# Optimization experiments

Hardware: AMD Instinct MI355X
Metric: run time of the kernel (lower is better)

The kernel has to match this reference:

```python
import jax, jax.numpy as jnp
import numpy as np

B = 32768
D_IN = 512
UNITS = 512


def setup_inputs() -> dict:
    key = jax.random.key(0)
    ks = jax.random.split(key, 12)
    s = 1.0 / np.sqrt(D_IN)
    sh = 1.0 / np.sqrt(UNITS)
    return {
        "inputs": jax.random.normal(ks[0], (B, D_IN), dtype=jnp.float32),
        "state": jax.random.normal(ks[1], (B, UNITS), dtype=jnp.float32),
        "att_score": jax.random.uniform(ks[2], (B, 1), dtype=jnp.float32),
        # update gate
        "Wu_x": jax.random.normal(ks[3], (D_IN, UNITS), dtype=jnp.float32) * s,
        "bu": jnp.zeros((UNITS,), dtype=jnp.float32),
        "Wu_h": jax.random.normal(ks[4], (UNITS, UNITS), dtype=jnp.float32) * sh,
        # reset gate
        "Wr_x": jax.random.normal(ks[5], (D_IN, UNITS), dtype=jnp.float32) * s,
        "br": jnp.zeros((UNITS,), dtype=jnp.float32),
        "Wr_h": jax.random.normal(ks[6], (UNITS, UNITS), dtype=jnp.float32) * sh,
        # candidate memory
        "Wc_x": jax.random.normal(ks[7], (D_IN, UNITS), dtype=jnp.float32) * s,
        "bc": jnp.zeros((UNITS,), dtype=jnp.float32),
        "Wc_h": jax.random.normal(ks[8], (UNITS, UNITS), dtype=jnp.float32) * sh,
    }


def reference(inputs, state, att_score, Wu_x, bu, Wu_h, Wr_x, br, Wr_h, Wc_x, bc, Wc_h):
    # u = sigmoid(Dense_act(x) + Dense_noact(h))
    u = jax.nn.sigmoid(inputs @ Wu_x + bu + state @ Wu_h)
    # r = sigmoid(Dense_act(x) + Dense_noact(h))
    r = jax.nn.sigmoid(inputs @ Wr_x + br + state @ Wr_h)
    # c = tanh(Dense_act(x) + r * Dense_noact(h))
    c = jnp.tanh(inputs @ Wc_x + bc + r * (state @ Wc_h))
    u_ = att_score * u  # [B,1] * [B,U] broadcast
    state_next = (1.0 - u_) * state + u_ * c
    return state_next
```

## Files before the change

### kernel.cpp

```cpp
#include <hip/hip_runtime.h>
#include <hip/hip_bf16.h>
#include <stdint.h>

#define B_ROWS 32768
#define DIM 512
#define THREADS 256
#define NKT 32
#define ASLOT 16384
#define LDS_TOTAL (3 * ASLOT)

typedef __attribute__((ext_vector_type(8))) __bf16 bf16x8;
typedef __attribute__((ext_vector_type(4))) float f32x4;
typedef __attribute__((ext_vector_type(4))) unsigned int uint4v;

__device__ static inline unsigned short f2bf(float f) {
    unsigned int u = __builtin_bit_cast(unsigned int, f);
    u += 0x7fffu + ((u >> 16) & 1u);
    return (unsigned short)(u >> 16);
}

__device__ static inline void load_lds_16B(const void* g, void* lds) {
    __builtin_amdgcn_global_load_lds(
        (const __attribute__((address_space(1))) unsigned int*)g,
        (__attribute__((address_space(3))) unsigned int*)lds,
        16, 0, 0);
}

__global__ void prep_weights(const float* __restrict__ Wu_x, const float* __restrict__ Wu_h,
                             const float* __restrict__ Wr_x, const float* __restrict__ Wr_h,
                             const float* __restrict__ Wc_x, const float* __restrict__ Wc_h,
                             unsigned short* __restrict__ Wt2) {
    __shared__ float tile[32][33];
    const int t = blockIdx.z;
    const int k0 = blockIdx.x * 32;
    const int n0 = blockIdx.y * 32;
    const float* Wx = (t == 0) ? Wu_x : (t == 1) ? Wr_x : Wc_x;
    const float* Wh = (t == 0) ? Wu_h : (t == 1) ? Wr_h : Wc_h;
    const int tid = threadIdx.x;
    const int c = tid & 31, r0 = tid >> 5;
#pragma unroll
    for (int i = 0; i < 4; ++i) {
        int kl = r0 + i * 8;
        int k = k0 + kl;
        int n = n0 + c;
        float v = (k < 512) ? Wx[(size_t)k * 512 + n] : Wh[(size_t)(k - 512) * 512 + n];
        tile[kl][c] = v;
    }
    __syncthreads();
    const int kt = k0 >> 5;
#pragma unroll
    for (int i = 0; i < 4; ++i) {
        int nl = r0 + i * 8;
        int kc = c;
        int n = n0 + nl;
        Wt2[(((size_t)kt * 3 + t) * 512 + n) * 32 + kc] = f2bf(tile[kc][nl]);
    }
}

__global__ __launch_bounds__(THREADS, 2) void augru_main(
    const float* __restrict__ x, const float* __restrict__ h,
    const float* __restrict__ att, const unsigned short* __restrict__ Wt2,
    const float* __restrict__ bu, const float* __restrict__ br,
    const float* __restrict__ bc, float* __restrict__ out) {
    extern __shared__ char smem[];
    const int tid = threadIdx.x;
    const int lane = tid & 63;
    const int wid = tid >> 6;
    const int wm = wid >> 1;
    const int wn = wid & 1;
    const int id = blockIdx.x;
    const int wg = (id & 7) * 256 + (id >> 3);
    const int nb = wg & 7;
    const int mb = wg >> 3;
    const int cl = lane & 15;
    const int kg = lane >> 4;

    f32x4 accU[4][2], accR[4][2], accCx[4][2], accCh[4][2];
#pragma unroll
    for (int i = 0; i < 4; ++i)
#pragma unroll
        for (int j = 0; j < 2; ++j) {
            accU[i][j] = (f32x4)(0.f);
            accR[i][j] = (f32x4)(0.f);
            accCx[i][j] = (f32x4)(0.f);
            accCh[i][j] = (f32x4)(0.f);
        }

    const int arow_l = lane >> 3;
    const int ag = lane & 7;
    const unsigned aoffBase =
        (unsigned)(mb * 128 + wid * 32 + arow_l) * 2048
        + (unsigned)((ag * 16) ^ (arow_l << 4));
    auto stageA = [&](int slot, int ktn) {
        const char* bp = (ktn < 16) ? (const char*)x : (const char*)h;
        const unsigned ko = (unsigned)(ktn & 15) * 128;
        char* ldsb = smem + slot * ASLOT + wid * 4096;
#pragma unroll
        for (int q = 0; q < 4; ++q)
            load_lds_16B(bp + aoffBase + q * 16384 + ko, ldsb + q * 1024);
    };

    const char* gW = (const char*)Wt2
        + (size_t)((nb * 64 + wn * 32 + cl) * 64 + kg * 16);
    bf16x8 bbA[3][2], bbB[3][2];
    auto loadW = [&](bf16x8(&dst)[3][2], int ktn) {
        const char* p = gW + (size_t)ktn * 98304;
#pragma unroll
        for (int t = 0; t < 3; ++t)
#pragma unroll
            for (int ni = 0; ni < 2; ++ni)
                dst[t][ni] = *(const bf16x8*)(p + t * 32768 + ni * 1024);
    };

    auto cvt2 = [](float lo, float hi) {
        unsigned int r;
        asm("v_cvt_pk_bf16_f32 %0, %1, %2" : "=v"(r) : "v"(lo), "v"(hi));
        return r;
    };

    const int s7 = cl & 7;
    const int aRd1 = (wm * 64 + cl) * 128 + (((kg * 2) ^ s7) * 16);
    const int aRd2 = (wm * 64 + cl) * 128 + (((kg * 2 + 1) ^ s7) * 16);
    auto readA = [&](int slot, int mi) {
        const char* p = smem + slot * ASLOT + mi * 2048;
        f32x4 lo = *(const f32x4*)(p + aRd1);
        f32x4 hi = *(const f32x4*)(p + aRd2);
        uint4v q;
        q.x = cvt2(lo[0], lo[1]); q.y = cvt2(lo[2], lo[3]);
        q.z = cvt2(hi[0], hi[1]); q.w = cvt2(hi[2], hi[3]);
        return __builtin_bit_cast(bf16x8, q);
    };

    stageA(0, 0);
    stageA(1, 1);
    loadW(bbA, 0);

    auto body = [&](int kt, bf16x8(&cur)[3][2], bf16x8(&nxt)[3][2],
                    f32x4(&accC)[4][2]) {
        asm volatile("s_waitcnt vmcnt(0)" ::: "memory");
        __builtin_amdgcn_s_barrier();
        if (kt + 2 < NKT) stageA((kt + 2) % 3, kt + 2);
        if (kt + 1 < NKT) loadW(nxt, kt + 1);
        __builtin_amdgcn_sched_barrier(0);
        const int slot = kt % 3;
        bf16x8 a[4];
#pragma unroll
        for (int mi = 0; mi < 4; ++mi)
            a[mi] = readA(slot, mi);
        __builtin_amdgcn_s_setprio(1);
#pragma unroll
        for (int ni = 0; ni < 2; ++ni) {
#pragma unroll
            for (int mi = 0; mi < 4; ++mi)
                accU[mi][ni] = __builtin_amdgcn_mfma_f32_16x16x32_bf16(
                    a[mi], cur[0][ni], accU[mi][ni], 0, 0, 0);
#pragma unroll
            for (int mi = 0; mi < 4; ++mi)
                accR[mi][ni] = __builtin_amdgcn_mfma_f32_16x16x32_bf16(
                    a[mi], cur[1][ni], accR[mi][ni], 0, 0, 0);
#pragma unroll
            for (int mi = 0; mi < 4; ++mi)
                accC[mi][ni] = __builtin_amdgcn_mfma_f32_16x16x32_bf16(
                    a[mi], cur[2][ni], accC[mi][ni], 0, 0, 0);
        }
        __builtin_amdgcn_s_setprio(0);
    };

    body(0, bbA, bbB, accCx);  body(1, bbB, bbA, accCx);
    body(2, bbA, bbB, accCx);  body(3, bbB, bbA, accCx);
    body(4, bbA, bbB, accCx);  body(5, bbB, bbA, accCx);
    body(6, bbA, bbB, accCx);  body(7, bbB, bbA, accCx);
    body(8, bbA, bbB, accCx);  body(9, bbB, bbA, accCx);
    body(10, bbA, bbB, accCx); body(11, bbB, bbA, accCx);
    body(12, bbA, bbB, accCx); body(13, bbB, bbA, accCx);
    body(14, bbA, bbB, accCx); body(15, bbB, bbA, accCx);
    body(16, bbA, bbB, accCh); body(17, bbB, bbA, accCh);
    body(18, bbA, bbB, accCh); body(19, bbB, bbA, accCh);
    body(20, bbA, bbB, accCh); body(21, bbB, bbA, accCh);
    body(22, bbA, bbB, accCh); body(23, bbB, bbA, accCh);
    body(24, bbA, bbB, accCh); body(25, bbB, bbA, accCh);
    body(26, bbA, bbB, accCh); body(27, bbB, bbA, accCh);
    body(28, bbA, bbB, accCh); body(29, bbB, bbA, accCh);
    body(30, bbA, bbB, accCh); body(31, bbB, bbA, accCh);

#pragma unroll
    for (int ni = 0; ni < 2; ++ni) {
        const int col = nb * 64 + wn * 32 + ni * 16 + cl;
        const float bU = bu[col];
        const float bR = br[col];
        const float bC = bc[col];
#pragma unroll
        for (int mi = 0; mi < 4; ++mi) {
#pragma unroll
            for (int j = 0; j < 4; ++j) {
                const int row = mb * 128 + wm * 64 + mi * 16 + kg * 4 + j;
                const float up = accU[mi][ni][j] + bU;
                const float rp = accR[mi][ni][j] + bR;
                const float u = 1.f / (1.f + __expf(-up));
                const float r = 1.f / (1.f + __expf(-rp));
                const float cpre = accCx[mi][ni][j] + bC + r * accCh[mi][ni][j];
                const float e = __expf(-2.f * cpre);
                const float cc = (1.f - e) / (1.f + e);
                const float aa = att[row];
                const float hv = h[(size_t)row * 512 + col];
                const float u_ = aa * u;
                out[(size_t)row * 512 + col] = (1.f - u_) * hv + u_ * cc;
            }
        }
    }
}

extern "C" void kernel_launch(void* const* d_in, const int* in_sizes, int n_in,
                              void* d_out, int out_size, void* d_ws, size_t ws_size,
                              hipStream_t stream) {
    const float* x    = (const float*)d_in[0];
    const float* h    = (const float*)d_in[1];
    const float* att  = (const float*)d_in[2];
    const float* Wu_x = (const float*)d_in[3];
    const float* bu   = (const float*)d_in[4];
    const float* Wu_h = (const float*)d_in[5];
    const float* Wr_x = (const float*)d_in[6];
    const float* br   = (const float*)d_in[7];
    const float* Wr_h = (const float*)d_in[8];
    const float* Wc_x = (const float*)d_in[9];
    const float* bc   = (const float*)d_in[10];
    const float* Wc_h = (const float*)d_in[11];
    unsigned short* Wt2 = (unsigned short*)d_ws;
    float* out = (float*)d_out;

    prep_weights<<<dim3(32, 16, 3), 256, 0, stream>>>(Wu_x, Wu_h, Wr_x, Wr_h, Wc_x, Wc_h, Wt2);

    hipFuncSetAttribute((const void*)augru_main,
                        hipFuncAttributeMaxDynamicSharedMemorySize, LDS_TOTAL);
    augru_main<<<dim3(2048), THREADS, LDS_TOTAL, stream>>>(
        x, h, att, Wt2, bu, br, bc, out);
}
```

Baseline: 158.8 us.

## Stage A tiles through registers, convert to bf16 before LDS write

The fp32 activation tiles are no longer copied straight into LDS with global_load_lds. Each thread now loads them into registers, converts them to bf16 once, and writes the bf16 data to a double-buffered LDS slot with a new swizzle. This halves LDS footprint and LDS read traffic, and removes the repeated per-wave fp32-to-bf16 conversion when reading A. In exchange it costs extra VGPRs for the in-flight loads, adds a register round trip, and reduces the pipeline depth from three stages to two.

```diff
diff --git a/kernel.cpp b/kernel.cpp
--- a/kernel.cpp
+++ b/kernel.cpp
@@ -6,8 +6,8 @@
 #define DIM 512
 #define THREADS 256
 #define NKT 32
-#define ASLOT 16384
-#define LDS_TOTAL (3 * ASLOT)
+#define ASLOT 8192
+#define LDS_TOTAL (2 * ASLOT)
 
 typedef __attribute__((ext_vector_type(8))) __bf16 bf16x8;
 typedef __attribute__((ext_vector_type(4))) float f32x4;
@@ -17,13 +17,6 @@
     unsigned int u = __builtin_bit_cast(unsigned int, f);
     u += 0x7fffu + ((u >> 16) & 1u);
     return (unsigned short)(u >> 16);
-}
-
-__device__ static inline void load_lds_16B(const void* g, void* lds) {
-    __builtin_amdgcn_global_load_lds(
-        (const __attribute__((address_space(1))) unsigned int*)g,
-        (__attribute__((address_space(3))) unsigned int*)lds,
-        16, 0, 0);
 }
 
 __global__ void prep_weights(const float* __restrict__ Wu_x, const float* __restrict__ Wu_h,
@@ -86,30 +79,43 @@
             accCh[i][j] = (f32x4)(0.f);
         }
 
-    const int arow_l = lane >> 3;
-    const int ag = lane & 7;
-    const unsigned aoffBase =
-        (unsigned)(mb * 128 + wid * 32 + arow_l) * 2048
-        + (unsigned)((ag * 16) ^ (arow_l << 4));
-    auto stageA = [&](int slot, int ktn) {
-        const char* bp = (ktn < 16) ? (const char*)x : (const char*)h;
-        const unsigned ko = (unsigned)(ktn & 15) * 128;
-        char* ldsb = smem + slot * ASLOT + wid * 4096;
-#pragma unroll
-        for (int q = 0; q < 4; ++q)
-            load_lds_16B(bp + aoffBase + q * 16384 + ko, ldsb + q * 1024);
+    const int rowb = wm * 64 + cl;
+    const int aBase = rowb * 64 + ((kg * 16) ^ (((rowb >> 1) & 3) << 4));
+
+    const int arow = tid >> 1;
+    const int ap = tid & 1;
+    const int asw = ((arow >> 1) & 3) << 4;
+    const int dsA0 = arow * 64 + ((ap * 32) ^ asw);
+    const int dsA1 = arow * 64 + ((ap * 32 + 16) ^ asw);
+    const float* pAx = x + (size_t)(mb * 128 + arow) * 512 + ap * 16;
+    const float* pAh = h + (size_t)(mb * 128 + arow) * 512 - 512 + ap * 16;
+
+    f32x4 fa[4];
+    auto issueA = [&](int ktn) {
+        const float* g = ((ktn < 16) ? pAx : pAh) + ktn * 32;
+        asm volatile(
+            "global_load_dwordx4 %0, %4, off\n\t"
+            "global_load_dwordx4 %1, %4, off offset:16\n\t"
+            "global_load_dwordx4 %2, %4, off offset:32\n\t"
+            "global_load_dwordx4 %3, %4, off offset:48"
+            : "=&v"(fa[0]), "=&v"(fa[1]), "=&v"(fa[2]), "=&v"(fa[3])
+            : "v"(g)
+            : "memory");
     };
 
     const char* gW = (const char*)Wt2
         + (size_t)((nb * 64 + wn * 32 + cl) * 64 + kg * 16);
-    bf16x8 bbA[3][2], bbB[3][2];
     auto loadW = [&](bf16x8(&dst)[3][2], int ktn) {
         const char* p = gW + (size_t)ktn * 98304;
 #pragma unroll
-        for (int t = 0; t < 3; ++t)
-#pragma unroll
-            for (int ni = 0; ni < 2; ++ni)
-                dst[t][ni] = *(const bf16x8*)(p + t * 32768 + ni * 1024);
+        for (int t = 0; t < 3; ++t) {
+            asm volatile(
+                "global_load_dwordx4 %0, %2, off\n\t"
+                "global_load_dwordx4 %1, %2, off offset:1024"
+                : "=&v"(dst[t][0]), "=&v"(dst[t][1])
+                : "v"(p + t * 32768)
+                : "memory");
+        }
     };
 
     auto cvt2 = [](float lo, float hi) {
@@ -117,36 +123,40 @@
         asm("v_cvt_pk_bf16_f32 %0, %1, %2" : "=v"(r) : "v"(lo), "v"(hi));
         return r;
     };
-
-    const int s7 = cl & 7;
-    const int aRd1 = (wm * 64 + cl) * 128 + (((kg * 2) ^ s7) * 16);
-    const int aRd2 = (wm * 64 + cl) * 128 + (((kg * 2 + 1) ^ s7) * 16);
-    auto readA = [&](int slot, int mi) {
-        const char* p = smem + slot * ASLOT + mi * 2048;
-        f32x4 lo = *(const f32x4*)(p + aRd1);
-        f32x4 hi = *(const f32x4*)(p + aRd2);
-        uint4v q;
-        q.x = cvt2(lo[0], lo[1]); q.y = cvt2(lo[2], lo[3]);
-        q.z = cvt2(hi[0], hi[1]); q.w = cvt2(hi[2], hi[3]);
-        return __builtin_bit_cast(bf16x8, q);
-    };
-
-    stageA(0, 0);
-    stageA(1, 1);
+    auto convertA = [&](int slot) {
+        uint4v q0, q1;
+        q0.x = cvt2(fa[0][0], fa[0][1]); q0.y = cvt2(fa[0][2], fa[0][3]);
+        q0.z = cvt2(fa[1][0], fa[1][1]); q0.w = cvt2(fa[1][2], fa[1][3]);
+        q1.x = cvt2(fa[2][0], fa[2][1]); q1.y = cvt2(fa[2][2], fa[2][3]);
+        q1.z = cvt2(fa[3][0], fa[3][1]); q1.w = cvt2(fa[3][2], fa[3][3]);
+        char* base = smem + slot * ASLOT;
+        *(uint4v*)(base + dsA0) = q0;
+        *(uint4v*)(base + dsA1) = q1;
+    };
+
+    bf16x8 bbA[3][2], bbB[3][2];
+
+    issueA(0);
+    asm volatile("s_waitcnt vmcnt(0)" ::: "memory");
+    __builtin_amdgcn_sched_barrier(0);
+    convertA(0);
+    issueA(1);
     loadW(bbA, 0);
 
     auto body = [&](int kt, bf16x8(&cur)[3][2], bf16x8(&nxt)[3][2],
                     f32x4(&accC)[4][2]) {
-        asm volatile("s_waitcnt vmcnt(0)" ::: "memory");
+        asm volatile("s_waitcnt vmcnt(0) lgkmcnt(0)" ::: "memory");
+        __builtin_amdgcn_sched_barrier(0);
         __builtin_amdgcn_s_barrier();
-        if (kt + 2 < NKT) stageA((kt + 2) % 3, kt + 2);
+        if (kt + 1 < NKT) convertA((kt + 1) & 1);
+        if (kt + 2 < NKT) issueA(kt + 2);
         if (kt + 1 < NKT) loadW(nxt, kt + 1);
-        __builtin_amdgcn_sched_barrier(0);
-        const int slot = kt % 3;
+        const char* aS = smem + (kt & 1) * ASLOT;
         bf16x8 a[4];
 #pragma unroll
         for (int mi = 0; mi < 4; ++mi)
-            a[mi] = readA(slot, mi);
+            a[mi] = __builtin_bit_cast(bf16x8,
+                *(const uint4v*)(aS + aBase + mi * 1024));
         __builtin_amdgcn_s_setprio(1);
 #pragma unroll
         for (int ni = 0; ni < 2; ++ni) {
```

New measurement: 180.8 us. 1.14x slower.
